# Kernel tuning notes

Measured on AMD Instinct MI355X. Metric: run time of the kernel, lower is better.

## Reference

```python
import jax, jax.numpy as jnp
import numpy as np

NUM_HEADS = 8
WINDOW = 3
LOCAL_LEN = WINDOW * WINDOW
SR_RATIO = 8


def _normalize(v, eps=1e-12):
    n = jnp.linalg.norm(v, axis=-1, keepdims=True)
    return v / jnp.maximum(n, eps)


def _layernorm(v, g, b, eps=1e-5):
    m = v.mean(-1, keepdims=True)
    var = ((v - m) ** 2).mean(-1, keepdims=True)
    return (v - m) / jnp.sqrt(var + eps) * g + b


def _unfold3(x, H, W):
    # x: [B, C, H, W] -> [B, C, 9, H*W]  (kernel 3, pad 1, stride 1; torch nn.Unfold layout)
    B, C = x.shape[0], x.shape[1]
    xp = jnp.pad(x, ((0, 0), (0, 0), (1, 1), (1, 1)))
    patches = jnp.stack([xp[:, :, di:di + H, dj:dj + W]
                         for di in range(WINDOW) for dj in range(WINDOW)], axis=2)
    return patches.reshape(B, C, LOCAL_LEN, H * W)


def _forward(x, relative_coords_table, seq_length_scale, q_w, q_b, kv_w, kv_b,
             temperature, query_embedding, sr_w, sr_b, norm_g, norm_b,
             cpb_fc1_w, cpb_fc1_b, cpb_fc2_w, cpb_fc2_b,
             rel_bias_local, learnable_tokens, learnable_bias,
             proj_w, proj_b, relative_pos_index, padding_mask, H, W):
    B, N, C = x.shape
    hd = C // NUM_HEADS
    pool_H, pool_W = H // SR_RATIO, W // SR_RATIO
    pool_len = pool_H * pool_W

    # ---- queries ----
    q = (x @ q_w.T + q_b).reshape(B, N, NUM_HEADS, hd).transpose(0, 2, 1, 3)  # [B,h,N,d]
    q_norm = _normalize(q)
    q_scaled = (q_norm + query_embedding) * jax.nn.softplus(temperature) * seq_length_scale

    # ---- local k/v via unfold ----
    kv = x @ kv_w.T + kv_b  # [B,N,2C]
    k_loc = _normalize(kv[..., :C].reshape(B, N, NUM_HEADS, hd)).reshape(B, N, C)
    kv_img = jnp.concatenate([k_loc, kv[..., C:]], -1).transpose(0, 2, 1).reshape(B, 2 * C, H, W)
    kv_unf = _unfold3(kv_img, H, W).reshape(B, 2 * NUM_HEADS, hd, LOCAL_LEN, N)
    kv_unf = kv_unf.transpose(0, 1, 4, 2, 3)  # [B,2h,N,d,9]
    k_local, v_local = kv_unf[:, :NUM_HEADS], kv_unf[:, NUM_HEADS:]

    attn_local = jnp.einsum('bhnd,bhndl->bhnl', q_scaled, k_local) + rel_bias_local[:, None, :]
    attn_local = jnp.where(padding_mask, -jnp.inf, attn_local)

    # ---- pooled global k/v ----
    x_img = x.transpose(0, 2, 1).reshape(B, C, H, W)
    x_sr = jax.nn.gelu(jnp.einsum('oc,bchw->bohw', sr_w, x_img) + sr_b[None, :, None, None],
                       approximate=False)
    x_pool = x_sr.reshape(B, C, pool_H, SR_RATIO, pool_W, SR_RATIO).mean((3, 5))
    x_pool = x_pool.reshape(B, C, pool_len).transpose(0, 2, 1)
    x_pool = _layernorm(x_pool, norm_g, norm_b)
    kv_p = (x_pool @ kv_w.T + kv_b).reshape(B, pool_len, 2 * NUM_HEADS, hd).transpose(0, 2, 1, 3)
    k_pool, v_pool = kv_p[:, :NUM_HEADS], kv_p[:, NUM_HEADS:]

    # ---- continuous relative position bias (extrapolation path) ----
    cpb = jax.nn.relu(relative_coords_table @ cpb_fc1_w.T + cpb_fc1_b) @ cpb_fc2_w.T + cpb_fc2_b  # [T,h]
    pool_bias = cpb[relative_pos_index].reshape(N, pool_len, NUM_HEADS).transpose(2, 0, 1)  # [h,N,P]

    attn_pool = jnp.einsum('bhnd,bhpd->bhnp', q_scaled, _normalize(k_pool)) + pool_bias

    attn = jax.nn.softmax(jnp.concatenate([attn_local, attn_pool], -1), axis=-1)
    a_loc, a_pool = attn[..., :LOCAL_LEN], attn[..., LOCAL_LEN:]

    lt = jnp.einsum('bhnd,hdl->bhnl', q_norm, learnable_tokens) + learnable_bias + a_loc
    x_local = jnp.einsum('bhnl,bhndl->bhnd', lt, v_local)
    x_p = jnp.einsum('bhnp,bhpd->bhnd', a_pool, v_pool)
    out = (x_local + x_p).transpose(0, 2, 1, 3).reshape(B, N, C)
    return out @ proj_w.T + proj_b


def setup_inputs() -> dict:
    key = jax.random.key(0)
    B, H, W, C = 4, 64, 64, 256
    N = H * W
    hd = C // NUM_HEADS
    pool_H, pool_W = H // SR_RATIO, W // SR_RATIO
    pool_len = pool_H * pool_W

    # padding mask + per-query valid window length (get_seqlen_and_mask)
    ii, jj = np.meshgrid(np.arange(H), np.arange(W), indexing='ij')
    cols = []
    for di in range(WINDOW):
        for dj in range(WINDOW):
            ni, nj = ii + di - 1, jj + dj - 1
            cols.append(((ni < 0) | (ni >= H) | (nj < 0) | (nj >= W)).reshape(-1))
    padding_mask = np.stack(cols, -1)  # [N, 9], True = outside image
    local_len = (~padding_mask).sum(-1, keepdims=True).astype(np.float32)
    seq_length_scale = np.log(local_len + pool_len)  # [N, 1]

    # get_relative_position_cpb((H,W), (pool_H,pool_W))
    axis_q = np.arange(H, dtype=np.float64)
    axis_k = axis_q.reshape(pool_H, SR_RATIO).mean(-1)
    kh, kw = np.meshgrid(axis_k, axis_k, indexing='ij')
    qh, qw = np.meshgrid(axis_q, axis_q, indexing='ij')
    rel_h = (qh.ravel()[:, None] - kh.ravel()[None, :]) / (H - 1) * 8
    rel_w = (qw.ravel()[:, None] - kw.ravel()[None, :]) / (W - 1) * 8
    rel = np.stack([rel_h, rel_w], -1).reshape(-1, 2)
    table, idx = np.unique(rel, axis=0, return_inverse=True)
    table = np.sign(table) * np.log2(np.abs(table) + 1.0) / np.log2(8.0)

    ks = jax.random.split(key, 12)

    def nrm(k, shape, std=0.02):
        return jax.random.normal(k, shape, jnp.float32) * std

    return {
        'x': jax.random.normal(ks[0], (B, N, C), jnp.float32),
        'relative_coords_table': jnp.asarray(table, jnp.float32),
        'seq_length_scale': jnp.asarray(seq_length_scale, jnp.float32),
        'q_w': nrm(ks[1], (C, C)), 'q_b': jnp.zeros((C,), jnp.float32),
        'kv_w': nrm(ks[2], (2 * C, C)), 'kv_b': jnp.zeros((2 * C,), jnp.float32),
        'temperature': jnp.full((NUM_HEADS, 1, 1), float(np.log(np.expm1(1.0 / 0.24))), jnp.float32),
        'query_embedding': nrm(ks[3], (NUM_HEADS, 1, hd)),
        'sr_w': nrm(ks[4], (C, C)), 'sr_b': jnp.zeros((C,), jnp.float32),
        'norm_g': jnp.ones((C,), jnp.float32), 'norm_b': jnp.zeros((C,), jnp.float32),
        'cpb_fc1_w': nrm(ks[5], (512, 2), 0.1), 'cpb_fc1_b': jnp.zeros((512,), jnp.float32),
        'cpb_fc2_w': nrm(ks[6], (NUM_HEADS, 512)), 'cpb_fc2_b': jnp.zeros((NUM_HEADS,), jnp.float32),
        'rel_bias_local': nrm(ks[7], (NUM_HEADS, LOCAL_LEN), 0.0004),
        'learnable_tokens': nrm(ks[8], (NUM_HEADS, hd, LOCAL_LEN)),
        'learnable_bias': jnp.zeros((NUM_HEADS, 1, LOCAL_LEN), jnp.float32),
        'proj_w': nrm(ks[9], (C, C)), 'proj_b': jnp.zeros((C,), jnp.float32),
        'relative_pos_index': jnp.asarray(idx, jnp.int32),
        'padding_mask': jnp.asarray(padding_mask),
        'H': H, 'W': W,
    }


def reference(x, relative_coords_table, seq_length_scale, q_w, q_b, kv_w, kv_b,
              temperature, query_embedding, sr_w, sr_b, norm_g, norm_b,
              cpb_fc1_w, cpb_fc1_b, cpb_fc2_w, cpb_fc2_b,
              rel_bias_local, learnable_tokens, learnable_bias,
              proj_w, proj_b, relative_pos_index, padding_mask, H, W):
    return _forward(x, relative_coords_table, seq_length_scale, q_w, q_b, kv_w, kv_b,
                    temperature, query_embedding, sr_w, sr_b, norm_g, norm_b,
                    cpb_fc1_w, cpb_fc1_b, cpb_fc2_w, cpb_fc2_b,
                    rel_bias_local, learnable_tokens, learnable_bias,
                    proj_w, proj_b, relative_pos_index, padding_mask, H, W)
```

## Files before the change

kernel.cpp:

```cpp
#include <hip/hip_runtime.h>
#include <math.h>


typedef unsigned short ushort_t;
typedef __attribute__((ext_vector_type(8))) _Float16 half8;
typedef __attribute__((ext_vector_type(2))) _Float16 half2_t;
typedef __attribute__((ext_vector_type(4))) float f32x4;

static __device__ __forceinline__ ushort_t f2h(float f) {
    _Float16 h = (_Float16)f;
    return *(ushort_t*)&h;
}

static __device__ __forceinline__ float fdot2f(half2_t a, half2_t b, float c) {
#if __has_builtin(__builtin_amdgcn_fdot2)
    return __builtin_amdgcn_fdot2(a, b, c, false);
#else
    return (float)a[0] * (float)b[0] + (float)a[1] * (float)b[1] + c;
#endif
}

template <int CTRL>
static __device__ __forceinline__ float dpp_addf(float x) {
    int v = __builtin_amdgcn_update_dpp(
        0, __builtin_bit_cast(int, x), CTRL, 0xF, 0xF, true);
    return x + __builtin_bit_cast(float, v);
}
static __device__ __forceinline__ float quad_sumf(float x) {
    return dpp_addf<0x4E>(dpp_addf<0xB1>(x));
}
static __device__ __forceinline__ float sum16f(float x) {
    return dpp_addf<0x128>(dpp_addf<0x124>(quad_sumf(x)));
}

#define GLOAD16(g, l)                                                        \
    __builtin_amdgcn_global_load_lds(                                        \
        (const __attribute__((address_space(1))) unsigned int*)(g),          \
        (__attribute__((address_space(3))) unsigned int*)(l), 16, 0, 0)

template <int TM>
__global__ __launch_bounds__(256) void mfma_hgemm(
    const ushort_t* __restrict__ Ag, const ushort_t* __restrict__ Bg,
    const float* __restrict__ bias, float* __restrict__ out0,
    ushort_t* __restrict__ qh_out, ushort_t* __restrict__ kvh,
    ushort_t* __restrict__ xsrh, int mode)
{
    const int K = 256;
    const int IM = TM / 32;
    __shared__ ushort_t Ah[TM * 32];
    __shared__ ushort_t Bh[64 * 32];

    const int t = threadIdx.x;
    const int w = t >> 6;
    const int lane = t & 63;
    const int bm = blockIdx.y * TM;
    const int bn = blockIdx.x * 64;
    const int wm = (w >> 1) * (TM / 2);
    const int wn = (w & 1) * 32;

    f32x4 acc[IM][2];
#pragma unroll
    for (int i = 0; i < IM; ++i)
#pragma unroll
        for (int j = 0; j < 2; ++j) acc[i][j] = f32x4{0.f, 0.f, 0.f, 0.f};

    const int lrow = t >> 2;
    const int lk8  = (t & 3) * 8;

    for (int k0 = 0; k0 < K; k0 += 32) {
#pragma unroll
        for (int r = 0; r < TM / 64; ++r) {
            GLOAD16(Ag + (size_t)(bm + r * 64 + lrow) * K + k0 + lk8,
                    &Ah[(unsigned)(r * 64 + (w * 16)) * 32]);
        }
        GLOAD16(Bg + (size_t)(bn + lrow) * K + k0 + lk8,
                &Bh[(unsigned)(w * 16) * 32]);
        __syncthreads();

        const int fr = lane & 15;
        const int fq = (lane >> 4) * 8;
        half8 af[IM], bf[2];
#pragma unroll
        for (int i = 0; i < IM; ++i)
            af[i] = *(const half8*)&Ah[(wm + i * 16 + fr) * 32 + fq];
#pragma unroll
        for (int j = 0; j < 2; ++j)
            bf[j] = *(const half8*)&Bh[(wn + j * 16 + fr) * 32 + fq];
#pragma unroll
        for (int i = 0; i < IM; ++i)
#pragma unroll
            for (int j = 0; j < 2; ++j)
                acc[i][j] = __builtin_amdgcn_mfma_f32_16x16x32_f16(af[i], bf[j], acc[i][j], 0, 0, 0);
        __syncthreads();
    }

    const int fr = lane & 15;
    const int q4 = (lane >> 4) * 4;
#pragma unroll
    for (int i = 0; i < IM; ++i) {
#pragma unroll
        for (int r = 0; r < 4; ++r) {
            const int row = bm + wm + i * 16 + q4 + r;
            const int col0 = bn + wn + fr;
            const int col1 = col0 + 16;
            float v0 = acc[i][0][r] + bias[col0];
            float v1 = acc[i][1][r] + bias[col1];
            if (mode == 0) {
                if (col0 < 256) {
                    qh_out[(size_t)row * 256 + col0] = f2h(v0);
                    qh_out[(size_t)row * 256 + col1] = f2h(v1);
                } else if (col0 < 512) {
                    const float ss = sum16f(v0 * v0 + v1 * v1);
                    const float invn = 1.0f / fmaxf(sqrtf(ss), 1e-12f);
                    kvh[(size_t)row * 512 + (col0 - 256)] = f2h(v0 * invn);
                    kvh[(size_t)row * 512 + (col1 - 256)] = f2h(v1 * invn);
                } else if (col0 < 768) {
                    kvh[(size_t)row * 512 + (col0 - 256)] = f2h(v0);
                    kvh[(size_t)row * 512 + (col1 - 256)] = f2h(v1);
                } else {
                    v0 = 0.5f * v0 * (1.0f + erff(v0 * 0.70710678118654752f));
                    v1 = 0.5f * v1 * (1.0f + erff(v1 * 0.70710678118654752f));
                    xsrh[(size_t)row * 256 + (col0 - 768)] = f2h(v0);
                    xsrh[(size_t)row * 256 + (col1 - 768)] = f2h(v1);
                }
            } else if (mode == 2) {
                if (col0 < 256) {
                    const float ss = sum16f(v0 * v0 + v1 * v1);
                    const float invn = 1.0f / fmaxf(sqrtf(ss), 1e-12f);
                    v0 *= invn; v1 *= invn;
                }
                kvh[(size_t)row * 512 + col0] = f2h(v0);
                kvh[(size_t)row * 512 + col1] = f2h(v1);
            } else {
                out0[(size_t)row * 256 + col0] = v0;
                out0[(size_t)row * 256 + col1] = v1;
            }
        }
    }
}

__global__ __launch_bounds__(256) void prep_cpb(
    const float4* __restrict__ x, ushort4* __restrict__ xh, int n4, int nprep,
    const float* __restrict__ qw, const float* __restrict__ kvw,
    const float* __restrict__ srw, const float* __restrict__ pw,
    const float* __restrict__ qb, const float* __restrict__ kvb,
    const float* __restrict__ srb,
    ushort_t* __restrict__ Wall, ushort_t* __restrict__ Pw,
    float* __restrict__ ball,
    const float* __restrict__ table, const float* __restrict__ w1,
    const float* __restrict__ b1, const float* __restrict__ w2,
    const float* __restrict__ b2, float* __restrict__ outc, int T)
{
    if (blockIdx.x >= nprep) {
        const int wv = threadIdx.x >> 6;
        const int lane = threadIdx.x & 63;
        const int row = (blockIdx.x - nprep) * 4 + wv;
        if (row >= T) return;
        const float t0 = table[(size_t)row * 2];
        const float t1 = table[(size_t)row * 2 + 1];
        const int base = lane * 8;

        const float4* w1p = (const float4*)(w1 + (size_t)base * 2);
        float4 wa = w1p[0], wb = w1p[1], wc = w1p[2], wd = w1p[3];
        float4 ba = *(const float4*)(b1 + base);
        float4 bb = *(const float4*)(b1 + base + 4);
        float h[8];
        h[0] = fmaxf(fmaf(t1, wa.y, fmaf(t0, wa.x, ba.x)), 0.f);
        h[1] = fmaxf(fmaf(t1, wa.w, fmaf(t0, wa.z, ba.y)), 0.f);
        h[2] = fmaxf(fmaf(t1, wb.y, fmaf(t0, wb.x, ba.z)), 0.f);
        h[3] = fmaxf(fmaf(t1, wb.w, fmaf(t0, wb.z, ba.w)), 0.f);
        h[4] = fmaxf(fmaf(t1, wc.y, fmaf(t0, wc.x, bb.x)), 0.f);
        h[5] = fmaxf(fmaf(t1, wc.w, fmaf(t0, wc.z, bb.y)), 0.f);
        h[6] = fmaxf(fmaf(t1, wd.y, fmaf(t0, wd.x, bb.z)), 0.f);
        h[7] = fmaxf(fmaf(t1, wd.w, fmaf(t0, wd.z, bb.w)), 0.f);

#pragma unroll
        for (int hh = 0; hh < 8; ++hh) {
            const float4* w2p = (const float4*)(w2 + (size_t)hh * 512 + base);
            float4 p0 = w2p[0], p1 = w2p[1];
            float s = h[0]*p0.x + h[1]*p0.y + h[2]*p0.z + h[3]*p0.w
                    + h[4]*p1.x + h[5]*p1.y + h[6]*p1.z + h[7]*p1.w;
#pragma unroll
            for (int off = 1; off <= 32; off <<= 1) s += __shfl_xor(s, off);
            if (lane == 0) outc[(size_t)row * 8 + hh] = s + b2[hh];
        }
        return;
    }

    int idx = blockIdx.x * 256 + threadIdx.x;
    if (idx < n4) {
        float4 v = x[idx];
        ushort4 h;
        h.x = f2h(v.x); h.y = f2h(v.y); h.z = f2h(v.z); h.w = f2h(v.w);
        xh[idx] = h;
    }
    if (idx < 262144) {
        int nn = idx >> 8, k = idx & 255;
        float a;
        if (nn < 256)      a = qw[nn * 256 + k];
        else if (nn < 768) a = kvw[(nn - 256) * 256 + k];
        else               a = srw[(nn - 768) * 256 + k];
        Wall[idx] = f2h(a);
    }
    if (idx < 65536) Pw[idx] = f2h(pw[idx]);
    if (idx < 1024) {
        float bv;
        if (idx < 256)      bv = qb[idx];
        else if (idx < 768) bv = kvb[idx - 256];
        else                bv = srb[idx - 768];
        ball[idx] = bv;
    }
}

__global__ __launch_bounds__(256) void pool_ln(
    const ushort_t* __restrict__ xsr, const float* __restrict__ g,
    const float* __restrict__ be, ushort_t* __restrict__ xpool, int Hh, int Ww)
{
    const int C = 256;
    const int Nn = Hh * Ww;
    int b = blockIdx.x >> 6;
    int pidx = blockIdx.x & 63;
    int ph = pidx >> 3, pw = pidx & 7;
    int tid = threadIdx.x;
    float s = 0.f;
    for (int si = 0; si < 8; ++si) {
        int i = ph * 8 + si;
        const ushort_t* rowp = xsr + ((size_t)b * Nn + (size_t)i * Ww + pw * 8) * C + tid;
#pragma unroll
        for (int sj = 0; sj < 8; ++sj)
            s += (float)(*(const _Float16*)&rowp[(size_t)sj * C]);
    }
    s *= (1.f / 64.f);
    __shared__ float red[256];
    red[tid] = s; __syncthreads();
    for (int st = 128; st; st >>= 1) { if (tid < st) red[tid] += red[tid + st]; __syncthreads(); }
    float mean = red[0] * (1.f / 256.f);
    __syncthreads();
    float dv = s - mean;
    red[tid] = dv * dv; __syncthreads();
    for (int st = 128; st; st >>= 1) { if (tid < st) red[tid] += red[tid + st]; __syncthreads(); }
    float var = red[0] * (1.f / 256.f);
    xpool[(size_t)blockIdx.x * C + tid] = f2h(dv * rsqrtf(var + 1e-5f) * g[tid] + be[tid]);
}

__global__ __launch_bounds__(256) void attn_v8(
    const ushort_t* __restrict__ qh_g,
    const ushort_t* __restrict__ kvh,
    const ushort_t* __restrict__ kvph,
    const int* __restrict__ rpi,
    const float* __restrict__ cpbB,
    const float* __restrict__ sls, const float* __restrict__ temp,
    const float* __restrict__ qe, const float* __restrict__ rbl,
    const float* __restrict__ ltok, const float* __restrict__ lbias,
    ushort_t* __restrict__ attno_hf)
{
    const int h = blockIdx.y, b = blockIdx.z;
    const int t = threadIdx.x;
    const int i = blockIdx.x;

    __shared__ half8 kp_s[64][4];
    __shared__ half8 vp_s[64][4];
    __shared__ ushort_t pb_s[64][66];
    __shared__ float lts[9][32];
    __shared__ float rbl_s[9], lb_s[9], qe_s[32];

    {
        const int p = t >> 2;
        const int g4s = t & 3;
        const ushort_t* gk = kvph + ((size_t)(b * 64 + p)) * 512 + h * 32 + g4s * 8;
        kp_s[p][g4s] = *(const half8*)gk;
        vp_s[p][g4s] = *(const half8*)(gk + 256);
        const int rbase = i * 4096;
        for (int u = t; u < 4096; u += 256) {
            const int idx = rpi[rbase + u];
            pb_s[u >> 6][u & 63] = f2h(cpbB[(size_t)idx * 8 + h]);
        }
        for (int u = t; u < 288; u += 256) lts[u % 9][u / 9] = ltok[h * 288 + u];
        if (t < 9)  { rbl_s[t] = rbl[h * 9 + t]; lb_s[t] = lbias[h * 9 + t]; }
        if (t >= 64 && t < 96) qe_s[t - 64] = qe[h * 32 + (t - 64)];
    }
    __syncthreads();

    const int w = t >> 6;
    const int lane = t & 63;
    const int qi = lane >> 2;
    const int g4 = lane & 3;
    const int co = g4 * 8;
    const int j = w * 16 + qi;
    const int n = i * 64 + j;
    const size_t gq = (size_t)b * 4096 + n;

    const float tm = temp[h];
    const float sp = (tm > 20.f) ? tm : log1pf(expf(tm));

    float qv[8];
    {
        const half8 q8 = *(const half8*)(qh_g + gq * 256 + h * 32 + co);
        float ss = 0.f;
#pragma unroll
        for (int d = 0; d < 8; ++d) { qv[d] = (float)q8[d]; ss += qv[d] * qv[d]; }
        ss = quad_sumf(ss);
        const float invn = 1.0f / fmaxf(sqrtf(ss), 1e-12f);
#pragma unroll
        for (int d = 0; d < 8; ++d) qv[d] *= invn;
    }

    float lt[9];
#pragma unroll
    for (int l = 0; l < 9; ++l) {
        float dl = 0.f;
        const float4* lw = (const float4*)&lts[l][co];
#pragma unroll
        for (int c4 = 0; c4 < 2; ++c4) {
            float4 w4 = lw[c4];
            dl += qv[4*c4+0]*w4.x + qv[4*c4+1]*w4.y + qv[4*c4+2]*w4.z + qv[4*c4+3]*w4.w;
        }
        dl = quad_sumf(dl);
        lt[l] = dl + lb_s[l];
    }

    const float scal = sp * sls[n];
    half2_t qh[4];
#pragma unroll
    for (int c = 0; c < 4; ++c) {
        float a = (qv[2*c+0] + qe_s[co + 2*c+0]) * scal;
        float bq = (qv[2*c+1] + qe_s[co + 2*c+1]) * scal;
        qh[c] = half2_t{(_Float16)a, (_Float16)bq};
    }

    float sl[9];
#pragma unroll
    for (int l = 0; l < 9; ++l) {
        const int di = l / 3 - 1, dj = l % 3 - 1;
        const int ii = i + di;
        const int jn = j + dj;
        const bool ok = (ii >= 0) && (ii < 64) && (jn >= 0) && (jn < 64);
        const int ic = max(min(ii, 63), 0);
        const int jc = max(min(jn, 63), 0);
        const half8 k8 = *(const half8*)(kvh + ((size_t)(b * 4096 + ic * 64 + jc)) * 512 + h * 32 + co);
        float dk = 0.f;
        dk = fdot2f(qh[0], __builtin_shufflevector(k8, k8, 0, 1), dk);
        dk = fdot2f(qh[1], __builtin_shufflevector(k8, k8, 2, 3), dk);
        dk = fdot2f(qh[2], __builtin_shufflevector(k8, k8, 4, 5), dk);
        dk = fdot2f(qh[3], __builtin_shufflevector(k8, k8, 6, 7), dk);
        dk = quad_sumf(dk);
        sl[l] = ok ? (dk + rbl_s[l]) : -INFINITY;
    }

    float m = sl[0];
#pragma unroll
    for (int l = 1; l < 9; ++l) m = fmaxf(m, sl[l]);

    half2_t oh[4];
#pragma unroll
    for (int c = 0; c < 4; ++c) oh[c] = half2_t{(_Float16)0.f, (_Float16)0.f};
    float Z = 0.f;

    for (int cch = 0; cch < 8; ++cch) {
        float s8[8];
        float pbv[8];
#pragma unroll
        for (int c = 0; c < 4; ++c) {
            const half2_t p2 = *(const half2_t*)&pb_s[j][cch * 8 + 2 * c];
            pbv[2*c]   = (float)p2[0];
            pbv[2*c+1] = (float)p2[1];
        }
#pragma unroll
        for (int k = 0; k < 8; ++k) {
            const int p = cch * 8 + k;
            const half8 k8 = kp_s[p][g4];
            float acc = 0.f;
            acc = fdot2f(qh[0], __builtin_shufflevector(k8, k8, 0, 1), acc);
            acc = fdot2f(qh[1], __builtin_shufflevector(k8, k8, 2, 3), acc);
            acc = fdot2f(qh[2], __builtin_shufflevector(k8, k8, 4, 5), acc);
            acc = fdot2f(qh[3], __builtin_shufflevector(k8, k8, 6, 7), acc);
            acc = quad_sumf(acc);
            s8[k] = acc + pbv[k];
        }
        float cmax = s8[0];
#pragma unroll
        for (int k = 1; k < 8; ++k) cmax = fmaxf(cmax, s8[k]);
        const float m_new = fmaxf(m, cmax);
        const float factor = __expf(m - m_new);
        Z *= factor;
        const _Float16 fh = (_Float16)factor;
        const half2_t f2 = half2_t{fh, fh};
#pragma unroll
        for (int c = 0; c < 4; ++c) oh[c] *= f2;
        m = m_new;
#pragma unroll
        for (int k = 0; k < 8; ++k) {
            const float a = __expf(s8[k] - m);
            Z += a;
            const _Float16 ah = (_Float16)a;
            const half2_t a2 = half2_t{ah, ah};
            const half8 v8 = vp_s[cch * 8 + k][g4];
            oh[0] = a2 * __builtin_shufflevector(v8, v8, 0, 1) + oh[0];
            oh[1] = a2 * __builtin_shufflevector(v8, v8, 2, 3) + oh[1];
            oh[2] = a2 * __builtin_shufflevector(v8, v8, 4, 5) + oh[2];
            oh[3] = a2 * __builtin_shufflevector(v8, v8, 6, 7) + oh[3];
        }
    }

#pragma unroll
    for (int l = 0; l < 9; ++l) { sl[l] = __expf(sl[l] - m); Z += sl[l]; }

#pragma unroll
    for (int l = 0; l < 9; ++l) {
        const int di = l / 3 - 1, dj = l % 3 - 1;
        const int ii = i + di;
        const int jn = j + dj;
        const bool ok = (ii >= 0) && (ii < 64) && (jn >= 0) && (jn < 64);
        const int ic = max(min(ii, 63), 0);
        const int jc = max(min(jn, 63), 0);
        const float coef = ok ? (sl[l] + lt[l] * Z) : 0.f;
        const half8 v8 = *(const half8*)(kvh + ((size_t)(b * 4096 + ic * 64 + jc)) * 512 + 256 + h * 32 + co);
        const _Float16 ch = (_Float16)coef;
        const half2_t c2 = half2_t{ch, ch};
        oh[0] = c2 * __builtin_shufflevector(v8, v8, 0, 1) + oh[0];
        oh[1] = c2 * __builtin_shufflevector(v8, v8, 2, 3) + oh[1];
        oh[2] = c2 * __builtin_shufflevector(v8, v8, 4, 5) + oh[2];
        oh[3] = c2 * __builtin_shufflevector(v8, v8, 6, 7) + oh[3];
    }

    const float invZ = 1.0f / Z;
    ushort4* outp = (ushort4*)(attno_hf + gq * 256 + h * 32 + co);
#pragma unroll
    for (int c4 = 0; c4 < 2; ++c4) {
        ushort4 u;
        u.x = f2h((float)oh[2*c4+0][0] * invZ);
        u.y = f2h((float)oh[2*c4+0][1] * invZ);
        u.z = f2h((float)oh[2*c4+1][0] * invZ);
        u.w = f2h((float)oh[2*c4+1][1] * invZ);
        outp[c4] = u;
    }
}

extern "C" void kernel_launch(void* const* d_in, const int* in_sizes, int n_in,
                              void* d_out, int out_size, void* d_ws, size_t ws_size,
                              hipStream_t stream)
{
    const float* x    = (const float*)d_in[0];
    const float* tbl  = (const float*)d_in[1];
    const float* sls  = (const float*)d_in[2];
    const float* q_w  = (const float*)d_in[3];
    const float* q_b  = (const float*)d_in[4];
    const float* kv_w = (const float*)d_in[5];
    const float* kv_b = (const float*)d_in[6];
    const float* temp = (const float*)d_in[7];
    const float* qe   = (const float*)d_in[8];
    const float* sr_w = (const float*)d_in[9];
    const float* sr_b = (const float*)d_in[10];
    const float* ng   = (const float*)d_in[11];
    const float* nb   = (const float*)d_in[12];
    const float* f1w  = (const float*)d_in[13];
    const float* f1b  = (const float*)d_in[14];
    const float* f2w  = (const float*)d_in[15];
    const float* f2b  = (const float*)d_in[16];
    const float* rbl  = (const float*)d_in[17];
    const float* ltok = (const float*)d_in[18];
    const float* lbias= (const float*)d_in[19];
    const float* pw   = (const float*)d_in[20];
    const float* pb   = (const float*)d_in[21];
    const int*   rpi  = (const int*)d_in[22];

    const int C = 256, Hh = 64, Ww = 64, Nn = Hh * Ww;
    const int B = in_sizes[0] / (Nn * C);
    const int T = in_sizes[1] / 2;
    const int M = B * Nn;

    float* ws = (float*)d_ws;
    size_t o = 0;
    ushort_t* qh    = (ushort_t*)(ws + o); o += (size_t)M * C / 2;
    ushort_t* kvh   = (ushort_t*)(ws + o); o += (size_t)M * C;
    ushort_t* xsrh  = (ushort_t*)(ws + o); o += (size_t)M * C / 2;
    ushort_t* xpoolh= (ushort_t*)(ws + o); o += (size_t)B * 64 * C / 2;
    ushort_t* kvph  = (ushort_t*)(ws + o); o += (size_t)B * 64 * C;
    float* cpbB  = ws + o; o += (size_t)T * 8;
    ushort_t* xh   = (ushort_t*)(ws + o); o += (size_t)M * C / 2;
    ushort_t* Wall = (ushort_t*)(ws + o); o += 1024 * 256 / 2;
    ushort_t* Pwh  = (ushort_t*)(ws + o); o += 256 * 256 / 2;
    float* ball = ws + o; o += 1024;
    ushort_t* attno_hf = xh;

    dim3 blk(256);
    const int n4x = M * C / 4;
    const int nprep = (n4x + 255) / 256;
    const int ncpb  = (T + 3) / 4;

    prep_cpb<<<nprep + ncpb, blk, 0, stream>>>(
        (const float4*)x, (ushort4*)xh, n4x, nprep,
        q_w, kv_w, sr_w, pw, q_b, kv_b, sr_b, Wall, Pwh, ball,
        tbl, f1w, f1b, f2w, f2b, cpbB, T);
    mfma_hgemm<128><<<dim3(16, M / 128), blk, 0, stream>>>(
        xh, Wall, ball, nullptr, qh, kvh, xsrh, 0);
    pool_ln<<<B * 64, blk, 0, stream>>>(xsrh, ng, nb, xpoolh, Hh, Ww);
    mfma_hgemm<64><<<dim3(8, (B * 64) / 64), blk, 0, stream>>>(
        xpoolh, Wall + 256 * 256, ball + 256, nullptr, nullptr, kvph, nullptr, 2);
    attn_v8<<<dim3(64, 8, B), blk, 0, stream>>>(
        qh, kvh, kvph, rpi, cpbB, sls, temp, qe, rbl, ltok, lbias, attno_hf);
    mfma_hgemm<64><<<dim3(4, M / 64), blk, 0, stream>>>(
        attno_hf, Pwh, pb, (float*)d_out, nullptr, nullptr, nullptr, 1);
}
```

Before: 214.5 us.

## Double-buffer GEMM LDS tiles, swizzle layout, and widen N tile for QKV GEMM

Reworks the MFMA GEMM to double-buffer the A/B shared-memory tiles, so the global-to-LDS load of the next K slice overlaps the MFMAs on the current one, leaving one barrier per iteration. It also XOR-swizzles the 8-element K chunks in LDS to cut bank conflicts on fragment reads. The tile width becomes a template parameter, and the first projection GEMM uses 128x128 tiles (half the blocks, more MFMAs per wave). The cost is doubled LDS use and more accumulator registers, which may lower occupancy or leave too few blocks for the GPU's CUs.

```diff
diff --git a/kernel.cpp b/kernel.cpp
--- a/kernel.cpp
+++ b/kernel.cpp
@@ -38,7 +38,7 @@
         (const __attribute__((address_space(1))) unsigned int*)(g),          \
         (__attribute__((address_space(3))) unsigned int*)(l), 16, 0, 0)
 
-template <int TM>
+template <int TM, int TN>
 __global__ __launch_bounds__(256) void mfma_hgemm(
     const ushort_t* __restrict__ Ag, const ushort_t* __restrict__ Bg,
     const float* __restrict__ bias, float* __restrict__ out0,
@@ -47,93 +47,108 @@
 {
     const int K = 256;
     const int IM = TM / 32;
-    __shared__ ushort_t Ah[TM * 32];
-    __shared__ ushort_t Bh[64 * 32];
+    const int JN = TN / 32;
+    __shared__ ushort_t Ah[2][TM * 32];
+    __shared__ ushort_t Bh[2][TN * 32];
 
     const int t = threadIdx.x;
     const int w = t >> 6;
     const int lane = t & 63;
     const int bm = blockIdx.y * TM;
-    const int bn = blockIdx.x * 64;
+    const int bn = blockIdx.x * TN;
     const int wm = (w >> 1) * (TM / 2);
-    const int wn = (w & 1) * 32;
-
-    f32x4 acc[IM][2];
+    const int wn = (w & 1) * (TN / 2);
+
+    f32x4 acc[IM][JN];
 #pragma unroll
     for (int i = 0; i < IM; ++i)
 #pragma unroll
-        for (int j = 0; j < 2; ++j) acc[i][j] = f32x4{0.f, 0.f, 0.f, 0.f};
-
-    const int lrow = t >> 2;
-    const int lk8  = (t & 3) * 8;
-
+        for (int j = 0; j < JN; ++j) acc[i][j] = f32x4{0.f, 0.f, 0.f, 0.f};
+
+    const int lrow  = t >> 2;
+    const int lk8sw = ((t & 3) ^ ((t >> 3) & 3)) * 8;
+
+#define STAGE(bufi, k0s)                                                     \
+    do {                                                                     \
+        _Pragma("unroll")                                                    \
+        for (int r = 0; r < TM / 64; ++r)                                    \
+            GLOAD16(Ag + (size_t)(bm + r * 64 + lrow) * K + (k0s) + lk8sw,   \
+                    &Ah[bufi][(unsigned)(r * 64 + w * 16) * 32]);            \
+        _Pragma("unroll")                                                    \
+        for (int r = 0; r < TN / 64; ++r)                                    \
+            GLOAD16(Bg + (size_t)(bn + r * 64 + lrow) * K + (k0s) + lk8sw,   \
+                    &Bh[bufi][(unsigned)(r * 64 + w * 16) * 32]);            \
+    } while (0)
+
+    const int fr   = lane & 15;
+    const int sws8 = ((lane >> 4) ^ ((fr >> 1) & 3)) * 8;
+
+    STAGE(0, 0);
+    __syncthreads();
+    int buf = 0;
     for (int k0 = 0; k0 < K; k0 += 32) {
-#pragma unroll
-        for (int r = 0; r < TM / 64; ++r) {
-            GLOAD16(Ag + (size_t)(bm + r * 64 + lrow) * K + k0 + lk8,
-                    &Ah[(unsigned)(r * 64 + (w * 16)) * 32]);
-        }
-        GLOAD16(Bg + (size_t)(bn + lrow) * K + k0 + lk8,
-                &Bh[(unsigned)(w * 16) * 32]);
+        if (k0 + 32 < K) STAGE(buf ^ 1, k0 + 32);
+
+        half8 af[IM], bf[JN];
+#pragma unroll
+        for (int i = 0; i < IM; ++i)
+            af[i] = *(const half8*)&Ah[buf][(unsigned)(wm + i * 16 + fr) * 32 + sws8];
+#pragma unroll
+        for (int j = 0; j < JN; ++j)
+            bf[j] = *(const half8*)&Bh[buf][(unsigned)(wn + j * 16 + fr) * 32 + sws8];
+#pragma unroll
+        for (int i = 0; i < IM; ++i)
+#pragma unroll
+            for (int j = 0; j < JN; ++j)
+                acc[i][j] = __builtin_amdgcn_mfma_f32_16x16x32_f16(af[i], bf[j], acc[i][j], 0, 0, 0);
+
         __syncthreads();
-
-        const int fr = lane & 15;
-        const int fq = (lane >> 4) * 8;
-        half8 af[IM], bf[2];
-#pragma unroll
-        for (int i = 0; i < IM; ++i)
-            af[i] = *(const half8*)&Ah[(wm + i * 16 + fr) * 32 + fq];
-#pragma unroll
-        for (int j = 0; j < 2; ++j)
-            bf[j] = *(const half8*)&Bh[(wn + j * 16 + fr) * 32 + fq];
-#pragma unroll
-        for (int i = 0; i < IM; ++i)
-#pragma unroll
-            for (int j = 0; j < 2; ++j)
-                acc[i][j] = __builtin_amdgcn_mfma_f32_16x16x32_f16(af[i], bf[j], acc[i][j], 0, 0, 0);
-        __syncthreads();
-    }
-
-    const int fr = lane & 15;
+        buf ^= 1;
+    }
+#undef STAGE
+
     const int q4 = (lane >> 4) * 4;
 #pragma unroll
     for (int i = 0; i < IM; ++i) {
 #pragma unroll
-        for (int r = 0; r < 4; ++r) {
-            const int row = bm + wm + i * 16 + q4 + r;
-            const int col0 = bn + wn + fr;
-            const int col1 = col0 + 16;
-            float v0 = acc[i][0][r] + bias[col0];
-            float v1 = acc[i][1][r] + bias[col1];
-            if (mode == 0) {
-                if (col0 < 256) {
-                    qh_out[(size_t)row * 256 + col0] = f2h(v0);
-                    qh_out[(size_t)row * 256 + col1] = f2h(v1);
-                } else if (col0 < 512) {
-                    const float ss = sum16f(v0 * v0 + v1 * v1);
-                    const float invn = 1.0f / fmaxf(sqrtf(ss), 1e-12f);
-                    kvh[(size_t)row * 512 + (col0 - 256)] = f2h(v0 * invn);
-                    kvh[(size_t)row * 512 + (col1 - 256)] = f2h(v1 * invn);
-                } else if (col0 < 768) {
-                    kvh[(size_t)row * 512 + (col0 - 256)] = f2h(v0);
-                    kvh[(size_t)row * 512 + (col1 - 256)] = f2h(v1);
+        for (int jp = 0; jp < JN / 2; ++jp) {
+#pragma unroll
+            for (int r = 0; r < 4; ++r) {
+                const int row = bm + wm + i * 16 + q4 + r;
+                const int col0 = bn + wn + jp * 32 + fr;
+                const int col1 = col0 + 16;
+                float v0 = acc[i][2 * jp][r] + bias[col0];
+                float v1 = acc[i][2 * jp + 1][r] + bias[col1];
+                if (mode == 0) {
+                    if (col0 < 256) {
+                        qh_out[(size_t)row * 256 + col0] = f2h(v0);
+                        qh_out[(size_t)row * 256 + col1] = f2h(v1);
+                    } else if (col0 < 512) {
+                        const float ss = sum16f(v0 * v0 + v1 * v1);
+                        const float invn = 1.0f / fmaxf(sqrtf(ss), 1e-12f);
+                        kvh[(size_t)row * 512 + (col0 - 256)] = f2h(v0 * invn);
+                        kvh[(size_t)row * 512 + (col1 - 256)] = f2h(v1 * invn);
+                    } else if (col0 < 768) {
+                        kvh[(size_t)row * 512 + (col0 - 256)] = f2h(v0);
+                        kvh[(size_t)row * 512 + (col1 - 256)] = f2h(v1);
+                    } else {
+                        v0 = 0.5f * v0 * (1.0f + erff(v0 * 0.70710678118654752f));
+                        v1 = 0.5f * v1 * (1.0f + erff(v1 * 0.70710678118654752f));
+                        xsrh[(size_t)row * 256 + (col0 - 768)] = f2h(v0);
+                        xsrh[(size_t)row * 256 + (col1 - 768)] = f2h(v1);
+                    }
+                } else if (mode == 2) {
+                    if (col0 < 256) {
+                        const float ss = sum16f(v0 * v0 + v1 * v1);
+                        const float invn = 1.0f / fmaxf(sqrtf(ss), 1e-12f);
+                        v0 *= invn; v1 *= invn;
+                    }
+                    kvh[(size_t)row * 512 + col0] = f2h(v0);
+                    kvh[(size_t)row * 512 + col1] = f2h(v1);
                 } else {
-                    v0 = 0.5f * v0 * (1.0f + erff(v0 * 0.70710678118654752f));
-                    v1 = 0.5f * v1 * (1.0f + erff(v1 * 0.70710678118654752f));
-                    xsrh[(size_t)row * 256 + (col0 - 768)] = f2h(v0);
-                    xsrh[(size_t)row * 256 + (col1 - 768)] = f2h(v1);
+                    out0[(size_t)row * 256 + col0] = v0;
+                    out0[(size_t)row * 256 + col1] = v1;
                 }
-            } else if (mode == 2) {
-                if (col0 < 256) {
-                    const float ss = sum16f(v0 * v0 + v1 * v1);
-                    const float invn = 1.0f / fmaxf(sqrtf(ss), 1e-12f);
-                    v0 *= invn; v1 *= invn;
-                }
-                kvh[(size_t)row * 512 + col0] = f2h(v0);
-                kvh[(size_t)row * 512 + col1] = f2h(v1);
-            } else {
-                out0[(size_t)row * 256 + col0] = v0;
-                out0[(size_t)row * 256 + col1] = v1;
             }
         }
     }
@@ -489,16 +504,16 @@
     const int ncpb  = (T + 3) / 4;
 
     prep_cpb<<<nprep + ncpb, blk, 0, stream>>>(
-        (const float4*)x, (ushort4*)xh, n4x, nprep,
-        q_w, kv_w, sr_w, pw, q_b, kv_b, sr_b, Wall, Pwh, ball,
+        (const float4*)x, (ushort4*)xh, n4x,
+        nprep, q_w, kv_w, sr_w, pw, q_b, kv_b, sr_b, Wall, Pwh, ball,
         tbl, f1w, f1b, f2w, f2b, cpbB, T);
-    mfma_hgemm<128><<<dim3(16, M / 128), blk, 0, stream>>>(
+    mfma_hgemm<128, 128><<<dim3(8, M / 128), blk, 0, stream>>>(
         xh, Wall, ball, nullptr, qh, kvh, xsrh, 0);
     pool_ln<<<B * 64, blk, 0, stream>>>(xsrh, ng, nb, xpoolh, Hh, Ww);
-    mfma_hgemm<64><<<dim3(8, (B * 64) / 64), blk, 0, stream>>>(
+    mfma_hgemm<64, 64><<<dim3(8, (B * 64) / 64), blk, 0, stream>>>(
         xpoolh, Wall + 256 * 256, ball + 256, nullptr, nullptr, kvph, nullptr, 2);
     attn_v8<<<dim3(64, 8, B), blk, 0, stream>>>(
         qh, kvh, kvph, rpi, cpbB, sls, temp, qe, rbl, ltok, lbias, attno_hf);
-    mfma_hgemm<64><<<dim3(4, M / 64), blk, 0, stream>>>(
+    mfma_hgemm<64, 64><<<dim3(4, M / 64), blk, 0, stream>>>(
         attno_hf, Pwh, pb, (float*)d_out, nullptr, nullptr, nullptr, 1);
 }
```

After: 229.1 us. 1.07x slower.
